# Optimization experiments

Measured on AMD Instinct MI355X. Metric: run time of the kernel, lower is better.

Reference implementation:

```python
import jax, jax.numpy as jnp
import numpy as np

N_NODES = 50000
N_EDGES = 1200000
IN_DIM = 128
EDGE_DIM = 64
EMBED_DIM = 64
NUM_HEADS = 8


def segment_softmax(logits, segment_ids, num_segments):
    # numerically stable softmax over segments (receivers)
    mx = jax.ops.segment_max(logits, segment_ids, num_segments)
    e = jnp.exp(logits - mx[segment_ids])
    denom = jax.ops.segment_sum(e, segment_ids, num_segments)
    return e / denom[segment_ids]


def mish(x):
    return x * jnp.tanh(jax.nn.softplus(x))


def setup_inputs() -> dict:
    key = jax.random.key(0)
    ks = jax.random.split(key, 8)
    node_features = jax.random.normal(ks[0], (N_NODES, IN_DIM), dtype=jnp.float32)
    edge_features = jax.random.normal(ks[1], (N_EDGES, EDGE_DIM), dtype=jnp.float32)
    global_features = jax.random.normal(ks[2], (32,), dtype=jnp.float32)
    senders = jax.random.randint(ks[3], (N_EDGES,), 0, N_NODES, dtype=jnp.int32)
    receivers = jax.random.randint(ks[4], (N_EDGES,), 0, N_NODES, dtype=jnp.int32)
    W_kernel = jax.random.normal(ks[5], (IN_DIM, EMBED_DIM), dtype=jnp.float32) * (2.0 / (IN_DIM + EMBED_DIM)) ** 0.5
    W_bias = jnp.zeros((EMBED_DIM,), dtype=jnp.float32)
    We_kernel = jax.random.normal(ks[6], (EDGE_DIM, EMBED_DIM), dtype=jnp.float32) * (2.0 / (EDGE_DIM + EMBED_DIM)) ** 0.5
    We_bias = jnp.zeros((EMBED_DIM,), dtype=jnp.float32)
    a = jax.random.normal(ks[7], (NUM_HEADS, EMBED_DIM // NUM_HEADS), dtype=jnp.float32) * (2.0 / (NUM_HEADS + EMBED_DIM // NUM_HEADS)) ** 0.5
    return dict(node_features=node_features, edge_features=edge_features,
                global_features=global_features, senders=senders, receivers=receivers,
                W_kernel=W_kernel, W_bias=W_bias, We_kernel=We_kernel, We_bias=We_bias, a=a)


def reference(node_features, edge_features, global_features, senders, receivers,
              W_kernel, W_bias, We_kernel, We_bias, a):
    num_nodes = node_features.shape[0]
    H, D = a.shape  # num_heads, head_dim
    # share_weights=True: one Dense projects nodes for both send and recv roles
    nodes = node_features @ W_kernel + W_bias            # [N, H*D]
    send_edges = nodes[senders]                          # [E, H*D] gather
    recv_edges = nodes[receivers]                        # [E, H*D] gather
    x = send_edges + recv_edges + (edge_features @ We_kernel + We_bias)
    x = mish(x)
    xh = x.reshape(-1, H, D)                             # [E, H, D]
    attn_logits = jnp.sum(xh * a, axis=-1, keepdims=True)  # [E, H, 1]
    attn_weights = segment_softmax(attn_logits, receivers, num_nodes)  # [E, H, 1]
    edges = attn_weights * send_edges.reshape(-1, H, D)  # [E, H, D]
    edges = edges.reshape(-1, H * D)
    new_nodes = jax.ops.segment_sum(edges, receivers, num_nodes)  # [N, H*D]
    return new_nodes
```

## Files before the change

### kernel.cpp

```cpp
#include <hip/hip_runtime.h>
#include <math.h>

#define IN_DIM   128
#define EDGE_DIM 64
#define ED       64
#define NH       8
#define CAP      64
#define BKB      512
#define GMB      2048

typedef __attribute__((ext_vector_type(8))) __bf16 bf16x8;
typedef __attribute__((ext_vector_type(4))) __bf16 bf16x4;
typedef __attribute__((ext_vector_type(4))) float  f32x4;

__device__ __forceinline__ int atomInc(int* p) {
    return __hip_atomic_fetch_add(p, 1, __ATOMIC_RELAXED, __HIP_MEMORY_SCOPE_AGENT);
}

__device__ __forceinline__ float mish_f(float x) {
    float u  = __expf(fminf(x, 15.f));
    float nn = u * (u + 2.f);
    return x * __fdividef(nn, nn + 2.f);
}


__global__ __launch_bounds__(256) void node_proj(const float* __restrict__ nf,
                          const float* __restrict__ W,
                          const float* __restrict__ Wb,
                          __bf16* __restrict__ nodes_pf, int nN) {
    int lane = threadIdx.x & 63;
    int col  = lane & 15;
    int q    = lane >> 4;
    int wid    = blockIdx.x * 4 + (threadIdx.x >> 6);
    int nwaves = gridDim.x * 4;

    bf16x8 aw[4][4];
#pragma unroll
    for (int c = 0; c < 4; c++)
#pragma unroll
        for (int s = 0; s < 4; s++)
#pragma unroll
            for (int i = 0; i < 8; i++)
                aw[c][s][i] = (__bf16)W[(s * 32 + q * 8 + i) * ED + c * 16 + col];
    f32x4 wbv[4];
#pragma unroll
    for (int c = 0; c < 4; c++)
#pragma unroll
        for (int r = 0; r < 4; r++)
            wbv[c][r] = Wb[c * 16 + q * 4 + r];

    int ngroups = (nN + 15) >> 4;
    for (int g = wid; g < ngroups; g += nwaves) {
        int n = g * 16 + col;
        bool valid = (n < nN);
        long nb = (long)(valid ? n : nN - 1) * IN_DIM;
        bf16x8 bfr[4];
#pragma unroll
        for (int s = 0; s < 4; s++) {
            float4 f0 = *(const float4*)(nf + nb + s * 32 + q * 8);
            float4 f1 = *(const float4*)(nf + nb + s * 32 + q * 8 + 4);
            bfr[s][0] = (__bf16)f0.x; bfr[s][1] = (__bf16)f0.y;
            bfr[s][2] = (__bf16)f0.z; bfr[s][3] = (__bf16)f0.w;
            bfr[s][4] = (__bf16)f1.x; bfr[s][5] = (__bf16)f1.y;
            bfr[s][6] = (__bf16)f1.z; bfr[s][7] = (__bf16)f1.w;
        }
        f32x4 acc[4];
#pragma unroll
        for (int c = 0; c < 4; c++) {
            acc[c] = wbv[c];
#pragma unroll
            for (int s = 0; s < 4; s++)
                acc[c] = __builtin_amdgcn_mfma_f32_16x16x32_bf16(aw[c][s], bfr[s], acc[c], 0, 0, 0);
        }
        if (valid) {
            bf16x8 v01, v23;
#pragma unroll
            for (int i = 0; i < 8; i++) {
                v01[i] = (__bf16)acc[i >> 2][i & 3];
                v23[i] = (__bf16)acc[2 + (i >> 2)][i & 3];
            }
            *(bf16x8*)(nodes_pf + (long)n * ED + q * 16)     = v01;
            *(bf16x8*)(nodes_pf + (long)n * ED + q * 16 + 8) = v23;
        }
    }
}

__global__ __launch_bounds__(256) void gemm_bucket(
                           const float* __restrict__ ef,
                           const int* __restrict__ snd,
                           const int* __restrict__ rcv,
                           const __bf16* __restrict__ nodes_pf,
                           const float* __restrict__ We,
                           const float* __restrict__ Web,
                           const float* __restrict__ a,
                           __bf16* __restrict__ w8,
                           int* __restrict__ deg,
                           int2* __restrict__ buck, int nE) {
    if (blockIdx.x < BKB) {
        int i0 = blockIdx.x * 256 + threadIdx.x;
        for (int i = i0; i < nE; i += BKB * 256) {
            int r = rcv[i];
            int slot = atomInc(&deg[r]);
            if (slot < CAP) buck[(long)r * CAP + slot] = make_int2(i, snd[i]);
        }
        return;
    }
    int lane = threadIdx.x & 63;
    int col  = lane & 15;
    int q    = lane >> 4;
    int wid    = (blockIdx.x - BKB) * 4 + (threadIdx.x >> 6);
    int nwaves = GMB * 4;

    bf16x8 aw[4][2];
#pragma unroll
    for (int c = 0; c < 4; c++)
#pragma unroll
        for (int s = 0; s < 2; s++)
#pragma unroll
            for (int i = 0; i < 8; i++)
                aw[c][s][i] = (__bf16)We[(s * 32 + q * 8 + i) * ED + c * 16 + col];
    f32x4 wbv[4];
    float ahat[4][4];
#pragma unroll
    for (int c = 0; c < 4; c++)
#pragma unroll
        for (int r = 0; r < 4; r++) {
            int j = c * 16 + q * 4 + r;
            wbv[c][r]  = Web[j];
            ahat[c][r] = a[j];
        }

    int ngroups = (nE + 15) >> 4;
    for (int g = wid; g < ngroups; g += nwaves) {
        int e = g * 16 + col;
        bool valid = (e < nE);
        int ec = valid ? e : nE - 1;
        long eb = (long)ec * EDGE_DIM;
        bf16x8 bfr[2];
#pragma unroll
        for (int s = 0; s < 2; s++) {
            f32x4 f0 = __builtin_nontemporal_load((const f32x4*)(ef + eb + s * 32 + q * 8));
            f32x4 f1 = __builtin_nontemporal_load((const f32x4*)(ef + eb + s * 32 + q * 8 + 4));
            bfr[s][0] = (__bf16)f0[0]; bfr[s][1] = (__bf16)f0[1];
            bfr[s][2] = (__bf16)f0[2]; bfr[s][3] = (__bf16)f0[3];
            bfr[s][4] = (__bf16)f1[0]; bfr[s][5] = (__bf16)f1[1];
            bfr[s][6] = (__bf16)f1[2]; bfr[s][7] = (__bf16)f1[3];
        }
        int se = snd[ec], re = rcv[ec];
        bf16x8 s01 = *(const bf16x8*)(nodes_pf + (long)se * ED + q * 16);
        bf16x8 s23 = *(const bf16x8*)(nodes_pf + (long)se * ED + q * 16 + 8);
        bf16x8 r01 = *(const bf16x8*)(nodes_pf + (long)re * ED + q * 16);
        bf16x8 r23 = *(const bf16x8*)(nodes_pf + (long)re * ED + q * 16 + 8);

        f32x4 acc[4];
#pragma unroll
        for (int c = 0; c < 4; c++) {
            acc[c] = wbv[c];
            acc[c] = __builtin_amdgcn_mfma_f32_16x16x32_bf16(aw[c][0], bfr[0], acc[c], 0, 0, 0);
            acc[c] = __builtin_amdgcn_mfma_f32_16x16x32_bf16(aw[c][1], bfr[1], acc[c], 0, 0, 0);
        }
        float p[4];
#pragma unroll
        for (int c = 0; c < 4; c++) {
            float ph = 0.f;
#pragma unroll
            for (int r = 0; r < 4; r++) {
                float sv = (c < 2) ? (float)s01[c * 4 + r] : (float)s23[(c - 2) * 4 + r];
                float rv = (c < 2) ? (float)r01[c * 4 + r] : (float)r23[(c - 2) * 4 + r];
                float x = acc[c][r] + sv + rv;
                ph = fmaf(mish_f(x), ahat[c][r], ph);
            }
            p[c] = ph;
        }
        float w[4];
#pragma unroll
        for (int c = 0; c < 4; c++) {
            p[c] += __shfl_xor(p[c], 16);
            w[c] = __expf(p[c]);
        }
        if (valid) {
            if (q == 0) {
                bf16x4 v;
#pragma unroll
                for (int c = 0; c < 4; c++) v[c] = (__bf16)w[c];
                *(bf16x4*)(w8 + (long)e * NH) = v;
            } else if (q == 2) {
                bf16x4 v;
#pragma unroll
                for (int c = 0; c < 4; c++) v[c] = (__bf16)w[c];
                *(bf16x4*)(w8 + (long)e * NH + 4) = v;
            }
        }
    }
}

__global__ __launch_bounds__(256) void seg_sum(const int* __restrict__ deg,
                        const int2* __restrict__ buck,
                        const __bf16* __restrict__ w8,
                        const __bf16* __restrict__ nodes_pf,
                        float* __restrict__ out, int nN) {
    int rn = blockIdx.x * 4 + (threadIdx.x >> 6);
    if (rn >= nN) return;
    int j = threadIdx.x & 63;
    int qq = j >> 4, cc = (j >> 2) & 3, rr = j & 3;
    int f = cc * 16 + qq * 4 + rr;
    int h = f >> 3;
    int widx = (h & 1) * 4 + (h >> 1);
    int dg = min(deg[rn], CAP);
    long base = (long)rn * CAP;
    float acc = 0.f, dn = 0.f;
    for (int s0 = 0; s0 < dg; s0 += 8) {
        int2 b[8];
#pragma unroll
        for (int k = 0; k < 8; k++)
            b[k] = buck[base + min(s0 + k, dg - 1)];
        float wv[8], sv[8];
#pragma unroll
        for (int k = 0; k < 8; k++) {
            bool v = (s0 + k) < dg;
            wv[k] = v ? (float)w8[(long)b[k].x * NH + widx] : 0.f;
            sv[k] = (float)nodes_pf[(long)b[k].y * ED + j];
        }
#pragma unroll
        for (int k = 0; k < 8; k++) {
            acc = fmaf(wv[k], sv[k], acc);
            dn += wv[k];
        }
    }
    out[(long)rn * ED + f] = (dn > 0.f) ? __fdividef(acc, dn) : 0.f;
}

extern "C" void kernel_launch(void* const* d_in, const int* in_sizes, int n_in,
                              void* d_out, int out_size, void* d_ws, size_t ws_size,
                              hipStream_t stream) {
    const float* nf  = (const float*)d_in[0];
    const float* ef  = (const float*)d_in[1];
    const int*   snd = (const int*)d_in[3];
    const int*   rcv = (const int*)d_in[4];
    const float* W   = (const float*)d_in[5];
    const float* Wb  = (const float*)d_in[6];
    const float* We  = (const float*)d_in[7];
    const float* Web = (const float*)d_in[8];
    const float* a   = (const float*)d_in[9];

    int nN = in_sizes[0] / IN_DIM;
    int nE = in_sizes[3];
    float* out = (float*)d_out;

    __bf16* nodes_pf = (__bf16*)d_ws;
    __bf16* w8       = nodes_pf + (size_t)nN * ED;
    int*    deg      = (int*)(w8 + (size_t)nE * NH);
    int2*   buck     = (int2*)(deg + nN);

    hipMemsetAsync(deg, 0, (size_t)nN * sizeof(int), stream);

    node_proj<<<512, 256, 0, stream>>>(nf, W, Wb, nodes_pf, nN);
    gemm_bucket<<<BKB + GMB, 256, 0, stream>>>(ef, snd, rcv, nodes_pf, We, Web, a,
                                               w8, deg, buck, nE);
    seg_sum<<<(nN + 3) / 4, 256, 0, stream>>>(deg, buck, w8, nodes_pf, out, nN);
}
```

Baseline: 275.4 us.

## Merge node projection into edge GEMM kernel and move attention logits into segment sum

```diff
diff --git a/kernel.cpp b/kernel.cpp
--- a/kernel.cpp
+++ b/kernel.cpp
@@ -7,6 +7,7 @@
 #define NH       8
 #define CAP      64
 #define BKB      512
+#define NPB      512
 #define GMB      2048
 
 typedef __attribute__((ext_vector_type(8))) __bf16 bf16x8;
@@ -24,78 +25,24 @@
 }
 
 
-__global__ __launch_bounds__(256) void node_proj(const float* __restrict__ nf,
-                          const float* __restrict__ W,
-                          const float* __restrict__ Wb,
-                          __bf16* __restrict__ nodes_pf, int nN) {
+__global__ __launch_bounds__(256) void mega(
+                        const float* __restrict__ nf,
+                        const float* __restrict__ W,
+                        const float* __restrict__ Wb,
+                        const float* __restrict__ ef,
+                        const int* __restrict__ snd,
+                        const int* __restrict__ rcv,
+                        const float* __restrict__ We,
+                        const float* __restrict__ Web,
+                        __bf16* __restrict__ nodes_pf,
+                        __bf16* __restrict__ y,
+                        int* __restrict__ deg,
+                        int2* __restrict__ buck,
+                        int nN, int nE) {
     int lane = threadIdx.x & 63;
     int col  = lane & 15;
     int q    = lane >> 4;
-    int wid    = blockIdx.x * 4 + (threadIdx.x >> 6);
-    int nwaves = gridDim.x * 4;
-
-    bf16x8 aw[4][4];
-#pragma unroll
-    for (int c = 0; c < 4; c++)
-#pragma unroll
-        for (int s = 0; s < 4; s++)
-#pragma unroll
-            for (int i = 0; i < 8; i++)
-                aw[c][s][i] = (__bf16)W[(s * 32 + q * 8 + i) * ED + c * 16 + col];
-    f32x4 wbv[4];
-#pragma unroll
-    for (int c = 0; c < 4; c++)
-#pragma unroll
-        for (int r = 0; r < 4; r++)
-            wbv[c][r] = Wb[c * 16 + q * 4 + r];
-
-    int ngroups = (nN + 15) >> 4;
-    for (int g = wid; g < ngroups; g += nwaves) {
-        int n = g * 16 + col;
-        bool valid = (n < nN);
-        long nb = (long)(valid ? n : nN - 1) * IN_DIM;
-        bf16x8 bfr[4];
-#pragma unroll
-        for (int s = 0; s < 4; s++) {
-            float4 f0 = *(const float4*)(nf + nb + s * 32 + q * 8);
-            float4 f1 = *(const float4*)(nf + nb + s * 32 + q * 8 + 4);
-            bfr[s][0] = (__bf16)f0.x; bfr[s][1] = (__bf16)f0.y;
-            bfr[s][2] = (__bf16)f0.z; bfr[s][3] = (__bf16)f0.w;
-            bfr[s][4] = (__bf16)f1.x; bfr[s][5] = (__bf16)f1.y;
-            bfr[s][6] = (__bf16)f1.z; bfr[s][7] = (__bf16)f1.w;
-        }
-        f32x4 acc[4];
-#pragma unroll
-        for (int c = 0; c < 4; c++) {
-            acc[c] = wbv[c];
-#pragma unroll
-            for (int s = 0; s < 4; s++)
-                acc[c] = __builtin_amdgcn_mfma_f32_16x16x32_bf16(aw[c][s], bfr[s], acc[c], 0, 0, 0);
-        }
-        if (valid) {
-            bf16x8 v01, v23;
-#pragma unroll
-            for (int i = 0; i < 8; i++) {
-                v01[i] = (__bf16)acc[i >> 2][i & 3];
-                v23[i] = (__bf16)acc[2 + (i >> 2)][i & 3];
-            }
-            *(bf16x8*)(nodes_pf + (long)n * ED + q * 16)     = v01;
-            *(bf16x8*)(nodes_pf + (long)n * ED + q * 16 + 8) = v23;
-        }
-    }
-}
-
-__global__ __launch_bounds__(256) void gemm_bucket(
-                           const float* __restrict__ ef,
-                           const int* __restrict__ snd,
-                           const int* __restrict__ rcv,
-                           const __bf16* __restrict__ nodes_pf,
-                           const float* __restrict__ We,
-                           const float* __restrict__ Web,
-                           const float* __restrict__ a,
-                           __bf16* __restrict__ w8,
-                           int* __restrict__ deg,
-                           int2* __restrict__ buck, int nE) {
+
     if (blockIdx.x < BKB) {
         int i0 = blockIdx.x * 256 + threadIdx.x;
         for (int i = i0; i < nE; i += BKB * 256) {
@@ -105,10 +52,61 @@
         }
         return;
     }
-    int lane = threadIdx.x & 63;
-    int col  = lane & 15;
-    int q    = lane >> 4;
-    int wid    = (blockIdx.x - BKB) * 4 + (threadIdx.x >> 6);
+    if (blockIdx.x < BKB + NPB) {
+        int wid    = (blockIdx.x - BKB) * 4 + (threadIdx.x >> 6);
+        int nwaves = NPB * 4;
+        bf16x8 aw[4][4];
+#pragma unroll
+        for (int c = 0; c < 4; c++)
+#pragma unroll
+            for (int s = 0; s < 4; s++)
+#pragma unroll
+                for (int i = 0; i < 8; i++)
+                    aw[c][s][i] = (__bf16)W[(s * 32 + q * 8 + i) * ED + c * 16 + col];
+        f32x4 wbv[4];
+#pragma unroll
+        for (int c = 0; c < 4; c++)
+#pragma unroll
+            for (int r = 0; r < 4; r++)
+                wbv[c][r] = Wb[c * 16 + q * 4 + r];
+
+        int ngroups = (nN + 15) >> 4;
+        for (int g = wid; g < ngroups; g += nwaves) {
+            int n = g * 16 + col;
+            bool valid = (n < nN);
+            long nb = (long)(valid ? n : nN - 1) * IN_DIM;
+            bf16x8 bfr[4];
+#pragma unroll
+            for (int s = 0; s < 4; s++) {
+                float4 f0 = *(const float4*)(nf + nb + s * 32 + q * 8);
+                float4 f1 = *(const float4*)(nf + nb + s * 32 + q * 8 + 4);
+                bfr[s][0] = (__bf16)f0.x; bfr[s][1] = (__bf16)f0.y;
+                bfr[s][2] = (__bf16)f0.z; bfr[s][3] = (__bf16)f0.w;
+                bfr[s][4] = (__bf16)f1.x; bfr[s][5] = (__bf16)f1.y;
+                bfr[s][6] = (__bf16)f1.z; bfr[s][7] = (__bf16)f1.w;
+            }
+            f32x4 acc[4];
+#pragma unroll
+            for (int c = 0; c < 4; c++) {
+                acc[c] = wbv[c];
+#pragma unroll
+                for (int s = 0; s < 4; s++)
+                    acc[c] = __builtin_amdgcn_mfma_f32_16x16x32_bf16(aw[c][s], bfr[s], acc[c], 0, 0, 0);
+            }
+            if (valid) {
+                bf16x8 v01, v23;
+#pragma unroll
+                for (int i = 0; i < 8; i++) {
+                    v01[i] = (__bf16)acc[i >> 2][i & 3];
+                    v23[i] = (__bf16)acc[2 + (i >> 2)][i & 3];
+                }
+                *(bf16x8*)(nodes_pf + (long)n * ED + q * 16)     = v01;
+                *(bf16x8*)(nodes_pf + (long)n * ED + q * 16 + 8) = v23;
+            }
+        }
+        return;
+    }
+    int wid    = (blockIdx.x - BKB - NPB) * 4 + (threadIdx.x >> 6);
     int nwaves = GMB * 4;
 
     bf16x8 aw[4][2];
@@ -120,15 +118,11 @@
             for (int i = 0; i < 8; i++)
                 aw[c][s][i] = (__bf16)We[(s * 32 + q * 8 + i) * ED + c * 16 + col];
     f32x4 wbv[4];
-    float ahat[4][4];
 #pragma unroll
     for (int c = 0; c < 4; c++)
 #pragma unroll
-        for (int r = 0; r < 4; r++) {
-            int j = c * 16 + q * 4 + r;
-            wbv[c][r]  = Web[j];
-            ahat[c][r] = a[j];
-        }
+        for (int r = 0; r < 4; r++)
+            wbv[c][r] = Web[c * 16 + q * 4 + r];
 
     int ngroups = (nE + 15) >> 4;
     for (int g = wid; g < ngroups; g += nwaves) {
@@ -146,12 +140,6 @@
             bfr[s][4] = (__bf16)f1[0]; bfr[s][5] = (__bf16)f1[1];
             bfr[s][6] = (__bf16)f1[2]; bfr[s][7] = (__bf16)f1[3];
         }
-        int se = snd[ec], re = rcv[ec];
-        bf16x8 s01 = *(const bf16x8*)(nodes_pf + (long)se * ED + q * 16);
-        bf16x8 s23 = *(const bf16x8*)(nodes_pf + (long)se * ED + q * 16 + 8);
-        bf16x8 r01 = *(const bf16x8*)(nodes_pf + (long)re * ED + q * 16);
-        bf16x8 r23 = *(const bf16x8*)(nodes_pf + (long)re * ED + q * 16 + 8);
-
         f32x4 acc[4];
 #pragma unroll
         for (int c = 0; c < 4; c++) {
@@ -159,53 +147,32 @@
             acc[c] = __builtin_amdgcn_mfma_f32_16x16x32_bf16(aw[c][0], bfr[0], acc[c], 0, 0, 0);
             acc[c] = __builtin_amdgcn_mfma_f32_16x16x32_bf16(aw[c][1], bfr[1], acc[c], 0, 0, 0);
         }
-        float p[4];
-#pragma unroll
-        for (int c = 0; c < 4; c++) {
-            float ph = 0.f;
-#pragma unroll
-            for (int r = 0; r < 4; r++) {
-                float sv = (c < 2) ? (float)s01[c * 4 + r] : (float)s23[(c - 2) * 4 + r];
-                float rv = (c < 2) ? (float)r01[c * 4 + r] : (float)r23[(c - 2) * 4 + r];
-                float x = acc[c][r] + sv + rv;
-                ph = fmaf(mish_f(x), ahat[c][r], ph);
-            }
-            p[c] = ph;
-        }
-        float w[4];
-#pragma unroll
-        for (int c = 0; c < 4; c++) {
-            p[c] += __shfl_xor(p[c], 16);
-            w[c] = __expf(p[c]);
-        }
         if (valid) {
-            if (q == 0) {
-                bf16x4 v;
-#pragma unroll
-                for (int c = 0; c < 4; c++) v[c] = (__bf16)w[c];
-                *(bf16x4*)(w8 + (long)e * NH) = v;
-            } else if (q == 2) {
-                bf16x4 v;
-#pragma unroll
-                for (int c = 0; c < 4; c++) v[c] = (__bf16)w[c];
-                *(bf16x4*)(w8 + (long)e * NH + 4) = v;
-            }
-        }
-    }
-}
-
-__global__ __launch_bounds__(256) void seg_sum(const int* __restrict__ deg,
+            bf16x8 v01, v23;
+#pragma unroll
+            for (int i = 0; i < 8; i++) {
+                v01[i] = (__bf16)acc[i >> 2][i & 3];
+                v23[i] = (__bf16)acc[2 + (i >> 2)][i & 3];
+            }
+            *(bf16x8*)(y + (long)e * ED + q * 16)     = v01;
+            *(bf16x8*)(y + (long)e * ED + q * 16 + 8) = v23;
+        }
+    }
+}
+
+__global__ __launch_bounds__(256) void seg_fuse(const int* __restrict__ deg,
                         const int2* __restrict__ buck,
-                        const __bf16* __restrict__ w8,
+                        const __bf16* __restrict__ y,
                         const __bf16* __restrict__ nodes_pf,
+                        const float* __restrict__ a,
                         float* __restrict__ out, int nN) {
     int rn = blockIdx.x * 4 + (threadIdx.x >> 6);
     if (rn >= nN) return;
-    int j = threadIdx.x & 63;
-    int qq = j >> 4, cc = (j >> 2) & 3, rr = j & 3;
+    int p = threadIdx.x & 63;
+    int qq = p >> 4, cc = (p >> 2) & 3, rr = p & 3;
     int f = cc * 16 + qq * 4 + rr;
-    int h = f >> 3;
-    int widx = (h & 1) * 4 + (h >> 1);
+    float af = a[f];
+    float rv = (float)nodes_pf[(long)rn * ED + p];
     int dg = min(deg[rn], CAP);
     long base = (long)rn * CAP;
     float acc = 0.f, dn = 0.f;
@@ -214,17 +181,24 @@
 #pragma unroll
         for (int k = 0; k < 8; k++)
             b[k] = buck[base + min(s0 + k, dg - 1)];
-        float wv[8], sv[8];
+        float yv[8], sv[8];
 #pragma unroll
         for (int k = 0; k < 8; k++) {
-            bool v = (s0 + k) < dg;
-            wv[k] = v ? (float)w8[(long)b[k].x * NH + widx] : 0.f;
-            sv[k] = (float)nodes_pf[(long)b[k].y * ED + j];
+            yv[k] = (float)y[(long)b[k].x * ED + p];
+            sv[k] = (float)nodes_pf[(long)b[k].y * ED + p];
         }
 #pragma unroll
         for (int k = 0; k < 8; k++) {
-            acc = fmaf(wv[k], sv[k], acc);
-            dn += wv[k];
+            if (s0 + k < dg) {
+                float x = yv[k] + sv[k] + rv;
+                float pl = af * mish_f(x);
+                pl += __shfl_xor(pl, 1);
+                pl += __shfl_xor(pl, 2);
+                pl += __shfl_xor(pl, 16);
+                float w = __expf(pl);
+                acc = fmaf(w, sv[k], acc);
+                dn += w;
+            }
         }
     }
     out[(long)rn * ED + f] = (dn > 0.f) ? __fdividef(acc, dn) : 0.f;
@@ -248,14 +222,13 @@
     float* out = (float*)d_out;
 
     __bf16* nodes_pf = (__bf16*)d_ws;
-    __bf16* w8       = nodes_pf + (size_t)nN * ED;
-    int*    deg      = (int*)(w8 + (size_t)nE * NH);
+    __bf16* y        = nodes_pf + (size_t)nN * ED;
+    int*    deg      = (int*)(y + (size_t)nE * ED);
     int2*   buck     = (int2*)(deg + nN);
 
     hipMemsetAsync(deg, 0, (size_t)nN * sizeof(int), stream);
 
-    node_proj<<<512, 256, 0, stream>>>(nf, W, Wb, nodes_pf, nN);
-    gemm_bucket<<<BKB + GMB, 256, 0, stream>>>(ef, snd, rcv, nodes_pf, We, Web, a,
-                                               w8, deg, buck, nE);
-    seg_sum<<<(nN + 3) / 4, 256, 0, stream>>>(deg, buck, w8, nodes_pf, out, nN);
-}
+    mega<<<BKB + NPB + GMB, 256, 0, stream>>>(nf, W, Wb, ef, snd, rcv, We, Web,
+                                              nodes_pf, y, deg, buck, nN, nE);
+    seg_fuse<<<(nN + 3) / 4, 256, 0, stream>>>(deg, buck, y, nodes_pf, a, out, nN);
+}
```

Result: slower. 295.6 us (+7.3%).
